# Performance work log

Hardware: AMD Instinct MI355X
Metric: run time of the kernel (lower is better)

## Reference

```python
import jax, jax.numpy as jnp
import numpy as np

N = 100000   # nodes
E = 1600000  # edges
R = 500      # relation types
D = 128      # in_ent_feats == out_ent_feats
H = 8        # heads
Dh = 16      # head dim
DFF = 4 * D  # feed-forward hidden
HOPS = 5
ALPHA = 0.15
SLOPE = 0.2
EPS = 1e-5


def setup_inputs() -> dict:
    key = jax.random.key(0)
    ks = jax.random.split(key, 12)
    s = 0.05  # small-init scale
    return {
        "ent_feat": jax.random.normal(ks[0], (N, D), jnp.float32),
        "rel_feat": jax.random.normal(ks[1], (R, D), jnp.float32),
        "src": jax.random.randint(ks[2], (E,), 0, N),
        "dst": jax.random.randint(ks[3], (E,), 0, N),
        "e_type": jax.random.randint(ks[4], (E,), 0, R),
        "ln1_g": jnp.ones((D,), jnp.float32),
        "ln1_b": jnp.zeros((D,), jnp.float32),
        "W_ent": jax.random.normal(ks[5], (D, H * Dh), jnp.float32) * s,
        "W_rel": jax.random.normal(ks[6], (D, H * Dh), jnp.float32) * s,
        "attn_h": jax.random.normal(ks[7], (1, H, Dh), jnp.float32) * s,
        "attn_t": jax.random.normal(ks[8], (1, H, Dh), jnp.float32) * s,
        "attn_r": jax.random.normal(ks[9], (1, H, Dh), jnp.float32) * s,
        "ln2_g": jnp.ones((H * Dh,), jnp.float32),
        "ln2_b": jnp.zeros((H * Dh,), jnp.float32),
        "W1": jax.random.normal(ks[10], (H * Dh, DFF), jnp.float32) * s,
        "b1": jnp.zeros((DFF,), jnp.float32),
        "W2": jax.random.normal(ks[11], (DFF, H * Dh), jnp.float32) * s,
        "b2": jnp.zeros((H * Dh,), jnp.float32),
    }


def _ln(x, g, b):
    mu = x.mean(-1, keepdims=True)
    var = x.var(-1, keepdims=True)
    return (x - mu) * jax.lax.rsqrt(var + EPS) * g + b


def reference(ent_feat, rel_feat, src, dst, e_type,
              ln1_g, ln1_b, W_ent, W_rel, attn_h, attn_t, attn_r,
              ln2_g, ln2_b, W1, b1, W2, b2):
    # graph layer norm (dropout is identity at eval)
    h = _ln(ent_feat, ln1_g, ln1_b)                       # [N, D]
    feat = (h @ W_ent).reshape(N, H, Dh)                  # [N, H, Dh]
    frel = (rel_feat @ W_rel).reshape(R, H, Dh)           # [R, H, Dh]
    eh = (feat * attn_h).sum(-1)                          # [N, H]
    et = (feat * attn_t).sum(-1)                          # [N, H]
    er = (frel * attn_r).sum(-1)[e_type]                  # [E, H]
    # edge scores: u_add_v + relation term, leaky relu
    e = eh[src] + et[dst] + er                            # [E, H]
    e = jnp.where(e > 0, e, SLOPE * e)
    # edge softmax over incoming edges of each dst node
    m = jax.ops.segment_max(e, dst, num_segments=N)       # [N, H]
    ex = jnp.exp(e - m[dst])
    ssum = jax.ops.segment_sum(ex, dst, num_segments=N)
    a = ex / ssum[dst]                                    # [E, H]
    # PPR diffusion
    feat0 = feat
    f = feat0
    for _ in range(HOPS):
        msg = f[src] * a[:, :, None]                      # [E, H, Dh]
        agg = jax.ops.segment_sum(msg, dst, num_segments=N)
        f = (1.0 - ALPHA) * agg + ALPHA * feat0
    # residual (Identity since in == out)
    rst = f + h.reshape(N, H, Dh)
    rst = rst.reshape(N, H * Dh)
    # feed-forward sublayer with residual
    y = _ln(rst, ln2_g, ln2_b)
    ff = jax.nn.relu(y @ W1 + b1) @ W2 + b2
    return ff + rst
```

## Files before the change

### kernel.cpp

```cpp
#include <hip/hip_runtime.h>
#include <hip/hip_bf16.h>
#include <math.h>

#define N_NODES 100000
#define N_EDGES 1600000
#define N_REL   500
#define DIM     128
#define NHEAD   8
#define DFF     512
#define ALPHA   0.15f
#define SLOPE   0.2f
#define LN_EPS  1e-5f

#define SCHUNK   1024
#define NSCANBLK ((N_NODES + SCHUNK - 1) / SCHUNK)

typedef unsigned short u16;
typedef unsigned int   u32;

typedef __attribute__((ext_vector_type(8))) short  bf16x8;
typedef __attribute__((ext_vector_type(4))) float  f32x4;

__device__ __forceinline__ float bf2f(u16 u) {
    return __uint_as_float(((u32)u) << 16);
}
__device__ __forceinline__ u16 f2bf(float f) {
    __hip_bfloat16 b = __float2bfloat16(f);
    return *reinterpret_cast<u16*>(&b);
}
__device__ __forceinline__ u32 pack2(float a, float b) {
    return (u32)f2bf(a) | ((u32)f2bf(b) << 16);
}

__global__ void zero_k(int* __restrict__ p, int n) {
    int i = blockIdx.x * blockDim.x + threadIdx.x;
    if (i < n) p[i] = 0;
}

__global__ void swz1_k(const float* __restrict__ W1, u16* __restrict__ W1s) {
    const int i = blockIdx.x * 256 + threadIdx.x;
    const int k = i >> 9, n = i & 511;
    W1s[n * DIM + k] = f2bf(W1[i]);
}
__global__ void swz2_k(const float* __restrict__ W2, u16* __restrict__ W2s) {
    const int i = blockIdx.x * 256 + threadIdx.x;
    const int k = i >> 7, n = i & 127;
    W2s[n * DFF + k] = f2bf(W2[i]);
}
__global__ void swze_k(const float* __restrict__ W, u16* __restrict__ Ws) {
    const int i = blockIdx.x * 256 + threadIdx.x;
    const int k = i >> 7, n = i & 127;
    Ws[n * DIM + k] = f2bf(W[i]);
}

__global__ __launch_bounds__(128) void ln1_k(const float* __restrict__ x,
        const float* __restrict__ g, const float* __restrict__ b,
        float* __restrict__ h) {
    const int n = blockIdx.x, t = threadIdx.x;
    const float v = x[n * DIM + t];
    float s = v, q = v * v;
#pragma unroll
    for (int off = 32; off > 0; off >>= 1) {
        s += __shfl_xor(s, off, 64);
        q += __shfl_xor(q, off, 64);
    }
    __shared__ float ss[2], qq[2];
    if ((t & 63) == 0) { ss[t >> 6] = s; qq[t >> 6] = q; }
    __syncthreads();
    s = ss[0] + ss[1]; q = qq[0] + qq[1];
    const float mu  = s * (1.0f / 128.0f);
    const float var = q * (1.0f / 128.0f) - mu * mu;
    const float rs  = rsqrtf(fmaxf(var, 0.f) + LN_EPS);
    h[n * DIM + t] = (v - mu) * rs * g[t] + b[t];
}

#define HP 136
__global__ __launch_bounds__(256) void proj_k(const float* __restrict__ h,
        const u16* __restrict__ Wes,
        u16* __restrict__ feat0) {
    __shared__ u16 hsb[32 * HP];
    const int t   = threadIdx.x;
    const int n0b = blockIdx.x * 32;

    {
        const int sr = t >> 3;
        const int sc = (t & 7) * 16;
        const float* hrow = &h[(size_t)(n0b + sr) * DIM + sc];
        u16* drow = &hsb[sr * HP + sc];
#pragma unroll
        for (int i = 0; i < 4; ++i) {
            const float4 hv = ((const float4*)hrow)[i];
            ushort4 o;
            o.x = f2bf(hv.x); o.y = f2bf(hv.y); o.z = f2bf(hv.z); o.w = f2bf(hv.w);
            ((ushort4*)drow)[i] = o;
        }
    }
    __syncthreads();

    const int wv   = t >> 6;
    const int lane = t & 63;
    const int lm   = lane & 15;
    const int q4   = lane >> 4;
    const int mrow = (wv & 1) * 16;
    const int chalf = (wv >> 1) * 64;

    bf16x8 afr[4];
#pragma unroll
    for (int kt = 0; kt < 4; ++kt)
        afr[kt] = *(const bf16x8*)&hsb[(mrow + lm) * HP + kt * 32 + q4 * 8];

#pragma unroll
    for (int nt = 0; nt < 4; ++nt) {
        const int c0 = chalf + nt * 16;
        f32x4 acc = {0.f, 0.f, 0.f, 0.f};
#pragma unroll
        for (int kt = 0; kt < 4; ++kt) {
            const bf16x8 bfr = *(const bf16x8*)&Wes[(c0 + lm) * DIM + kt * 32 + q4 * 8];
            acc = __builtin_amdgcn_mfma_f32_16x16x32_bf16(afr[kt], bfr, acc, 0, 0, 0);
        }
#pragma unroll
        for (int r = 0; r < 4; ++r)
            feat0[(size_t)(n0b + mrow + q4 * 4 + r) * DIM + c0 + lm] = f2bf(acc[r]);
    }
}

__global__ __launch_bounds__(256) void eh_k(const u16* __restrict__ feat0,
        const float* __restrict__ attn_h, const float* __restrict__ attn_t,
        float* __restrict__ eh, float* __restrict__ et) {
    __shared__ float ahs[DIM], ats[DIM];
    const int t = threadIdx.x;
    if (t < DIM) { ahs[t] = attn_h[t]; ats[t] = attn_t[t]; }
    __syncthreads();
    const int idx  = blockIdx.x * 256 + t;
    const int n    = idx >> 3;
    const int head = idx & 7;
    const u16* fp = &feat0[(size_t)n * DIM + head * 16];
    float sh = 0.f, st = 0.f;
#pragma unroll
    for (int i = 0; i < 4; ++i) {
        const ushort4 f4 = ((const ushort4*)fp)[i];
        const int c = head * 16 + i * 4;
        sh += bf2f(f4.x) * ahs[c+0] + bf2f(f4.y) * ahs[c+1]
            + bf2f(f4.z) * ahs[c+2] + bf2f(f4.w) * ahs[c+3];
        st += bf2f(f4.x) * ats[c+0] + bf2f(f4.y) * ats[c+1]
            + bf2f(f4.z) * ats[c+2] + bf2f(f4.w) * ats[c+3];
    }
    eh[idx] = sh;
    et[idx] = st;
}

__global__ __launch_bounds__(128) void rel_k(const float* __restrict__ rel_feat,
        const float* __restrict__ W,
        const float* __restrict__ attn_r, float* __restrict__ er) {
    __shared__ float rf[DIM];
    __shared__ float pr[DIM];
    const int r = blockIdx.x, t = threadIdx.x;
    rf[t] = rel_feat[r * DIM + t];
    __syncthreads();
    float acc = 0.f;
    for (int d = 0; d < DIM; ++d) acc += rf[d] * W[d * DIM + t];
    pr[t] = acc * attn_r[t];
    __syncthreads();
    if (t < NHEAD) {
        float s = 0.f;
        for (int i = 0; i < 16; ++i) s += pr[t * 16 + i];
        er[r * NHEAD + t] = s;
    }
}

__global__ void count_k(const int* __restrict__ dst, int* __restrict__ counts) {
    int e = blockIdx.x * blockDim.x + threadIdx.x;
    if (e < N_EDGES) atomicAdd(&counts[dst[e]], 1);
}

__global__ __launch_bounds__(256) void scan1_k(const int* __restrict__ counts,
        int* __restrict__ offsets, int* __restrict__ blk_sums, int n) {
    __shared__ int wsum[4];
    const int t = threadIdx.x, lane = t & 63, wid = t >> 6;
    const int base = blockIdx.x * SCHUNK + t * 4;
    int v0 = 0, v1 = 0, v2 = 0, v3 = 0;
    if (base + 3 < n) {
        const int4 c4 = *(const int4*)&counts[base];
        v0 = c4.x; v1 = c4.y; v2 = c4.z; v3 = c4.w;
    } else {
        if (base + 0 < n) v0 = counts[base + 0];
        if (base + 1 < n) v1 = counts[base + 1];
        if (base + 2 < n) v2 = counts[base + 2];
        if (base + 3 < n) v3 = counts[base + 3];
    }
    const int s4 = v0 + v1 + v2 + v3;
    int incl = s4;
#pragma unroll
    for (int off = 1; off < 64; off <<= 1) {
        const int tt = __shfl_up(incl, off, 64);
        if (lane >= off) incl += tt;
    }
    if (lane == 63) wsum[wid] = incl;
    __syncthreads();
    int wbase = 0;
#pragma unroll
    for (int w = 0; w < 4; ++w) if (w < wid) wbase += wsum[w];
    const int excl = wbase + incl - s4;
    if (base + 0 < n) offsets[base + 0] = excl;
    if (base + 1 < n) offsets[base + 1] = excl + v0;
    if (base + 2 < n) offsets[base + 2] = excl + v0 + v1;
    if (base + 3 < n) offsets[base + 3] = excl + v0 + v1 + v2;
    if (t == 255) blk_sums[blockIdx.x] = wbase + incl;
}

__global__ __launch_bounds__(128) void scan2_k(const int* __restrict__ blk_sums,
        int* __restrict__ blk_off, int* __restrict__ offsets, int nblk, int n) {
    const int t = threadIdx.x;
    const int v = (t < nblk) ? blk_sums[t] : 0;
    int incl = v;
#pragma unroll
    for (int off = 1; off < 64; off <<= 1) {
        const int tt = __shfl_up(incl, off, 64);
        if ((t & 63) >= off) incl += tt;
    }
    __shared__ int w0sum;
    if (t == 63) w0sum = incl;
    __syncthreads();
    int x = incl - v;
    if (t >= 64) x += w0sum;
    if (t < nblk) blk_off[t] = x;
    if (t == nblk - 1) offsets[n] = x + v;
}

__global__ __launch_bounds__(256) void scan3_k(int* __restrict__ offsets,
        int* __restrict__ cursor, const int* __restrict__ blk_off, int n) {
    const int add  = blk_off[blockIdx.x];
    const int base = blockIdx.x * SCHUNK + threadIdx.x * 4;
#pragma unroll
    for (int j = 0; j < 4; ++j) {
        const int i = base + j;
        if (i < n) {
            const int o = offsets[i] + add;
            offsets[i] = o;
            cursor[i]  = o;
        }
    }
}

__global__ void scatter_k(const int* __restrict__ src, const int* __restrict__ dst,
        const int* __restrict__ etype,
        const float* __restrict__ eh, const float* __restrict__ et,
        const float* __restrict__ er,
        int* __restrict__ cursor, int* __restrict__ csr_src,
        u16* __restrict__ csr_ab) {
    const int e = blockIdx.x * blockDim.x + threadIdx.x;
    if (e >= N_EDGES) return;
    const int s = src[e], d = dst[e], r = etype[e];
    const float4 h0 = *(const float4*)&eh[s * NHEAD];
    const float4 h1 = *(const float4*)&eh[s * NHEAD + 4];
    const float4 t0 = *(const float4*)&et[d * NHEAD];
    const float4 t1 = *(const float4*)&et[d * NHEAD + 4];
    const float4 r0 = *(const float4*)&er[r * NHEAD];
    const float4 r1 = *(const float4*)&er[r * NHEAD + 4];
    float4 a0, a1;
    a0.x = h0.x + t0.x + r0.x; a0.y = h0.y + t0.y + r0.y;
    a0.z = h0.z + t0.z + r0.z; a0.w = h0.w + t0.w + r0.w;
    a1.x = h1.x + t1.x + r1.x; a1.y = h1.y + t1.y + r1.y;
    a1.z = h1.z + t1.z + r1.z; a1.w = h1.w + t1.w + r1.w;
    a0.x = a0.x > 0.f ? a0.x : SLOPE * a0.x;
    a0.y = a0.y > 0.f ? a0.y : SLOPE * a0.y;
    a0.z = a0.z > 0.f ? a0.z : SLOPE * a0.z;
    a0.w = a0.w > 0.f ? a0.w : SLOPE * a0.w;
    a1.x = a1.x > 0.f ? a1.x : SLOPE * a1.x;
    a1.y = a1.y > 0.f ? a1.y : SLOPE * a1.y;
    a1.z = a1.z > 0.f ? a1.z : SLOPE * a1.z;
    a1.w = a1.w > 0.f ? a1.w : SLOPE * a1.w;
    const int pos = atomicAdd(&cursor[d], 1);
    if (pos < 0 || pos >= N_EDGES) return;
    csr_src[pos] = s;
    uint4 packed;
    packed.x = pack2(a0.x, a0.y);
    packed.y = pack2(a0.z, a0.w);
    packed.z = pack2(a1.x, a1.y);
    packed.w = pack2(a1.z, a1.w);
    *(uint4*)&csr_ab[(size_t)pos * NHEAD] = packed;
}

__global__ __launch_bounds__(256) void softmax_k(const int* __restrict__ offsets,
        u16* __restrict__ csr_ab, float* __restrict__ inv_buf) {
    const int n = blockIdx.x * 4 + (threadIdx.x >> 6);
    const int beg = offsets[n], end = offsets[n + 1];
    const int lane = threadIdx.x & 63;
    const int k  = lane & 7;
    const int eo = lane >> 3;
    float m = -1e30f;
    for (int e = beg + eo; e < end; e += 8)
        m = fmaxf(m, bf2f(csr_ab[(size_t)e * NHEAD + k]));
    m = fmaxf(m, __shfl_xor(m, 8, 64));
    m = fmaxf(m, __shfl_xor(m, 16, 64));
    m = fmaxf(m, __shfl_xor(m, 32, 64));
    float ssum = 0.f;
    for (int e = beg + eo; e < end; e += 8) {
        const float ex = expf(bf2f(csr_ab[(size_t)e * NHEAD + k]) - m);
        csr_ab[(size_t)e * NHEAD + k] = f2bf(ex);
        ssum += ex;
    }
    ssum += __shfl_xor(ssum, 8, 64);
    ssum += __shfl_xor(ssum, 16, 64);
    ssum += __shfl_xor(ssum, 32, 64);
    const float inv = 1.f / fmaxf(ssum, 1e-20f);
    if (lane < 8) inv_buf[n * NHEAD + lane] = inv;
}

__global__ __launch_bounds__(256) void hop_k(const u16* f_in,
        u16* __restrict__ f_out, const u16* feat0,
        const int* __restrict__ offsets, const int* __restrict__ csr_src,
        const u16* __restrict__ csr_ab, const float* __restrict__ inv_buf) {
    const int n    = blockIdx.x * 4 + (threadIdx.x >> 6);
    const int lane = threadIdx.x & 63;
    const int beg = offsets[n], end = offsets[n + 1];
    const int hsel = lane >> 3;
    const int d2   = lane << 1;
    float2 acc = {0.f, 0.f};
    int e = beg;
    for (; e + 4 <= end; e += 4) {
        const int s0 = csr_src[e + 0];
        const int s1 = csr_src[e + 1];
        const int s2 = csr_src[e + 2];
        const int s3 = csr_src[e + 3];
        const float a0 = bf2f(csr_ab[(size_t)(e + 0) * NHEAD + hsel]);
        const float a1 = bf2f(csr_ab[(size_t)(e + 1) * NHEAD + hsel]);
        const float a2 = bf2f(csr_ab[(size_t)(e + 2) * NHEAD + hsel]);
        const float a3 = bf2f(csr_ab[(size_t)(e + 3) * NHEAD + hsel]);
        const ushort2 w0 = *(const ushort2*)&f_in[s0 * DIM + d2];
        const ushort2 w1 = *(const ushort2*)&f_in[s1 * DIM + d2];
        const ushort2 w2 = *(const ushort2*)&f_in[s2 * DIM + d2];
        const ushort2 w3 = *(const ushort2*)&f_in[s3 * DIM + d2];
        acc.x += a0 * bf2f(w0.x) + a1 * bf2f(w1.x) + a2 * bf2f(w2.x) + a3 * bf2f(w3.x);
        acc.y += a0 * bf2f(w0.y) + a1 * bf2f(w1.y) + a2 * bf2f(w2.y) + a3 * bf2f(w3.y);
    }
    for (; e < end; ++e) {
        const int s0 = csr_src[e];
        const float a0 = bf2f(csr_ab[(size_t)e * NHEAD + hsel]);
        const ushort2 w0 = *(const ushort2*)&f_in[s0 * DIM + d2];
        acc.x += a0 * bf2f(w0.x);
        acc.y += a0 * bf2f(w0.y);
    }
    const float iv = inv_buf[n * NHEAD + hsel];
    const ushort2 p = *(const ushort2*)&feat0[n * DIM + d2];
    const float ox = (1.f - ALPHA) * acc.x * iv + ALPHA * bf2f(p.x);
    const float oy = (1.f - ALPHA) * acc.y * iv + ALPHA * bf2f(p.y);
    ushort2 o; o.x = f2bf(ox); o.y = f2bf(oy);
    *(ushort2*)&f_out[n * DIM + d2] = o;
}

#define YP 136
#define ZP 520
__global__ __launch_bounds__(256) void ffn_k(const u16* __restrict__ f,
        const float* __restrict__ h,
        const float* __restrict__ g2, const float* __restrict__ b2ln,
        const u16* __restrict__ W1s,
        const float* __restrict__ b1,
        const u16* __restrict__ W2s,
        const float* __restrict__ b2,
        float* __restrict__ out) {
    __shared__ u16 ysb[32 * YP];
    __shared__ u16 zsb[32 * ZP];
    __shared__ float red[32][8];
    __shared__ float red2[32][8];
    __shared__ float mu_s[32], rs_s[32];

    const int t   = threadIdx.x;
    const int n0b = blockIdx.x * 32;

    const int an = t >> 3;
    const int ap = t & 7;
    float rv[16];
    {
        const int gbase = (n0b + an) * DIM + ap * 16;
#pragma unroll
        for (int i = 0; i < 4; ++i) {
            const ushort4 fu = *(const ushort4*)&f[gbase + i * 4];
            const float4  hv = *(const float4*)&h[gbase + i * 4];
            rv[i * 4 + 0] = bf2f(fu.x) + hv.x;
            rv[i * 4 + 1] = bf2f(fu.y) + hv.y;
            rv[i * 4 + 2] = bf2f(fu.z) + hv.z;
            rv[i * 4 + 3] = bf2f(fu.w) + hv.w;
        }
        float s = 0.f, q = 0.f;
#pragma unroll
        for (int i = 0; i < 16; ++i) { s += rv[i]; q += rv[i] * rv[i]; }
        red[an][ap] = s; red2[an][ap] = q;
    }
    __syncthreads();
    if (t < 32) {
        float s = 0.f, q = 0.f;
#pragma unroll
        for (int i = 0; i < 8; ++i) { s += red[t][i]; q += red2[t][i]; }
        const float mu  = s * (1.0f / 128.0f);
        const float var = q * (1.0f / 128.0f) - mu * mu;
        mu_s[t] = mu;
        rs_s[t] = rsqrtf(fmaxf(var, 0.f) + LN_EPS);
    }
    __syncthreads();
    {
        const float mu = mu_s[an], rs = rs_s[an];
#pragma unroll
        for (int i = 0; i < 4; ++i) {
            ushort4 yo;
            const int c = ap * 16 + i * 4;
            yo.x = f2bf((rv[i*4+0] - mu) * rs * g2[c+0] + b2ln[c+0]);
            yo.y = f2bf((rv[i*4+1] - mu) * rs * g2[c+1] + b2ln[c+1]);
            yo.z = f2bf((rv[i*4+2] - mu) * rs * g2[c+2] + b2ln[c+2]);
            yo.w = f2bf((rv[i*4+3] - mu) * rs * g2[c+3] + b2ln[c+3]);
            *(ushort4*)&ysb[an * YP + c] = yo;
        }
    }
    __syncthreads();

    const int wv   = t >> 6;
    const int lane = t & 63;
    const int lm   = lane & 15;
    const int q4   = lane >> 4;

    bf16x8 afr[2][4];
#pragma unroll
    for (int mt = 0; mt < 2; ++mt)
#pragma unroll
        for (int kt = 0; kt < 4; ++kt)
            afr[mt][kt] = *(const bf16x8*)&ysb[(mt * 16 + lm) * YP + kt * 32 + q4 * 8];

    for (int nt = 0; nt < 8; ++nt) {
        const int n0 = wv * 128 + nt * 16;
        f32x4 acc0 = {0.f, 0.f, 0.f, 0.f};
        f32x4 acc1 = {0.f, 0.f, 0.f, 0.f};
#pragma unroll
        for (int kt = 0; kt < 4; ++kt) {
            const bf16x8 bfr = *(const bf16x8*)&W1s[(n0 + lm) * DIM + kt * 32 + q4 * 8];
            acc0 = __builtin_amdgcn_mfma_f32_16x16x32_bf16(afr[0][kt], bfr, acc0, 0, 0, 0);
            acc1 = __builtin_amdgcn_mfma_f32_16x16x32_bf16(afr[1][kt], bfr, acc1, 0, 0, 0);
        }
        const float bias = b1[n0 + lm];
#pragma unroll
        for (int r = 0; r < 4; ++r) {
            zsb[(q4 * 4 + r) * ZP + n0 + lm]        = f2bf(fmaxf(acc0[r] + bias, 0.f));
            zsb[(16 + q4 * 4 + r) * ZP + n0 + lm]   = f2bf(fmaxf(acc1[r] + bias, 0.f));
        }
    }
    __syncthreads();

    f32x4 acc[2][2];
#pragma unroll
    for (int i = 0; i < 2; ++i)
#pragma unroll
        for (int j = 0; j < 2; ++j)
            acc[i][j] = (f32x4){0.f, 0.f, 0.f, 0.f};
    const int c0 = wv * 32;
    for (int kt = 0; kt < 16; ++kt) {
        const bf16x8 a0 = *(const bf16x8*)&zsb[(lm) * ZP + kt * 32 + q4 * 8];
        const bf16x8 a1 = *(const bf16x8*)&zsb[(16 + lm) * ZP + kt * 32 + q4 * 8];
        const bf16x8 b0 = *(const bf16x8*)&W2s[(c0 + lm) * DFF + kt * 32 + q4 * 8];
        const bf16x8 b1f = *(const bf16x8*)&W2s[(c0 + 16 + lm) * DFF + kt * 32 + q4 * 8];
        acc[0][0] = __builtin_amdgcn_mfma_f32_16x16x32_bf16(a0, b0, acc[0][0], 0, 0, 0);
        acc[0][1] = __builtin_amdgcn_mfma_f32_16x16x32_bf16(a0, b1f, acc[0][1], 0, 0, 0);
        acc[1][0] = __builtin_amdgcn_mfma_f32_16x16x32_bf16(a1, b0, acc[1][0], 0, 0, 0);
        acc[1][1] = __builtin_amdgcn_mfma_f32_16x16x32_bf16(a1, b1f, acc[1][1], 0, 0, 0);
    }

#pragma unroll
    for (int ntile = 0; ntile < 2; ++ntile) {
        const int col = c0 + ntile * 16 + lm;
        const float bias = b2[col];
#pragma unroll
        for (int mt = 0; mt < 2; ++mt) {
#pragma unroll
            for (int r = 0; r < 4; ++r) {
                const int row  = mt * 16 + q4 * 4 + r;
                const int gidx = (n0b + row) * DIM + col;
                out[gidx] = acc[mt][ntile][r] + bias + bf2f(f[gidx]) + h[gidx];
            }
        }
    }
}

extern "C" void kernel_launch(void* const* d_in, const int* in_sizes, int n_in,
                              void* d_out, int out_size, void* d_ws, size_t ws_size,
                              hipStream_t stream) {
    const float* ent_feat = (const float*)d_in[0];
    const float* rel_feat = (const float*)d_in[1];
    const int*   src      = (const int*)d_in[2];
    const int*   dst      = (const int*)d_in[3];
    const int*   e_type   = (const int*)d_in[4];
    const float* ln1_g    = (const float*)d_in[5];
    const float* ln1_b    = (const float*)d_in[6];
    const float* W_ent    = (const float*)d_in[7];
    const float* W_rel    = (const float*)d_in[8];
    const float* attn_h   = (const float*)d_in[9];
    const float* attn_t   = (const float*)d_in[10];
    const float* attn_r   = (const float*)d_in[11];
    const float* ln2_g    = (const float*)d_in[12];
    const float* ln2_b    = (const float*)d_in[13];
    const float* W1       = (const float*)d_in[14];
    const float* b1       = (const float*)d_in[15];
    const float* W2       = (const float*)d_in[16];
    const float* b2       = (const float*)d_in[17];
    float* out = (float*)d_out;

    char* ws = (char*)d_ws;
    size_t used = 0;
    auto alloc = [&](size_t bytes) -> char* {
        char* p = ws + used;
        used += (bytes + 255) & ~(size_t)255;
        return p;
    };
    float* h       = (float*)alloc((size_t)N_NODES * DIM * 4);
    u16*   feat0   = (u16*)  alloc((size_t)N_NODES * DIM * 2);
    u16*   fA      = (u16*)  alloc((size_t)N_NODES * DIM * 2);
    u16*   fB      = (u16*)  alloc((size_t)N_NODES * DIM * 2);
    u16*   csr_ab  = (u16*)  alloc((size_t)N_EDGES * NHEAD * 2);
    float* eh      = (float*)alloc((size_t)N_NODES * NHEAD * 4);
    float* et      = (float*)alloc((size_t)N_NODES * NHEAD * 4);
    float* inv_buf = (float*)alloc((size_t)N_NODES * NHEAD * 4);
    int*   csr_src = (int*)  alloc((size_t)N_EDGES * 4);
    int*   counts  = (int*)  alloc((size_t)N_NODES * 4);
    int*   offsets = (int*)  alloc((size_t)(N_NODES + 1) * 4);
    int*   cursor  = (int*)  alloc((size_t)N_NODES * 4);
    float* er      = (float*)alloc((size_t)N_REL * NHEAD * 4);
    u16*   W1s     = (u16*)  alloc((size_t)DIM * DFF * 2);
    u16*   W2s     = (u16*)  alloc((size_t)DFF * DIM * 2);
    u16*   Wes     = (u16*)  alloc((size_t)DIM * DIM * 2);
    int*   blk_sums= (int*)  alloc((size_t)NSCANBLK * 4);
    int*   blk_off = (int*)  alloc((size_t)NSCANBLK * 4);

    if (used > ws_size) return;

    swz1_k<<<DIM * DFF / 256, 256, 0, stream>>>(W1, W1s);
    swz2_k<<<DFF * DIM / 256, 256, 0, stream>>>(W2, W2s);
    swze_k<<<DIM * DIM / 256, 256, 0, stream>>>(W_ent, Wes);

    ln1_k<<<N_NODES, 128, 0, stream>>>(ent_feat, ln1_g, ln1_b, h);
    proj_k<<<N_NODES / 32, 256, 0, stream>>>(h, Wes, feat0);
    eh_k<<<N_NODES * NHEAD / 256, 256, 0, stream>>>(feat0, attn_h, attn_t, eh, et);
    rel_k<<<N_REL, 128, 0, stream>>>(rel_feat, W_rel, attn_r, er);

    zero_k<<<(N_NODES + 255) / 256, 256, 0, stream>>>(counts, N_NODES);
    count_k<<<(N_EDGES + 255) / 256, 256, 0, stream>>>(dst, counts);
    scan1_k<<<NSCANBLK, 256, 0, stream>>>(counts, offsets, blk_sums, N_NODES);
    scan2_k<<<1, 128, 0, stream>>>(blk_sums, blk_off, offsets, NSCANBLK, N_NODES);
    scan3_k<<<NSCANBLK, 256, 0, stream>>>(offsets, cursor, blk_off, N_NODES);
    scatter_k<<<(N_EDGES + 255) / 256, 256, 0, stream>>>(src, dst, e_type, eh, et, er,
                                                         cursor, csr_src, csr_ab);
    softmax_k<<<N_NODES / 4, 256, 0, stream>>>(offsets, csr_ab, inv_buf);

    hop_k<<<N_NODES / 4, 256, 0, stream>>>(feat0, fA, feat0, offsets, csr_src, csr_ab, inv_buf);
    hop_k<<<N_NODES / 4, 256, 0, stream>>>(fA, fB, feat0, offsets, csr_src, csr_ab, inv_buf);
    hop_k<<<N_NODES / 4, 256, 0, stream>>>(fB, fA, feat0, offsets, csr_src, csr_ab, inv_buf);
    hop_k<<<N_NODES / 4, 256, 0, stream>>>(fA, fB, feat0, offsets, csr_src, csr_ab, inv_buf);
    hop_k<<<N_NODES / 4, 256, 0, stream>>>(fB, fA, feat0, offsets, csr_src, csr_ab, inv_buf);

    ffn_k<<<N_NODES / 32, 256, 0, stream>>>(fA, h, ln2_g, ln2_b, W1s, b1, W2s, b2,
                                            out);
}
```

Measured before the change: 954.7 us.

## Store LN1 output as bf16 and move edge score computation into softmax

The layer-norm output h is now written as bf16 rather than fp32, which halves its traffic in the projection and FFN kernels but rounds the residual added at the end. The scatter kernel now only writes edge ids into CSR order. The softmax kernel gathers src, etype, eh and er per edge, recomputing the scores in both passes, and writes csr_src. This drops the scattered 16-byte score writes from scatter but adds indirect gathers, read twice, in softmax.

```diff
diff --git a/kernel.cpp b/kernel.cpp
--- a/kernel.cpp
+++ b/kernel.cpp
@@ -28,9 +28,6 @@
     __hip_bfloat16 b = __float2bfloat16(f);
     return *reinterpret_cast<u16*>(&b);
 }
-__device__ __forceinline__ u32 pack2(float a, float b) {
-    return (u32)f2bf(a) | ((u32)f2bf(b) << 16);
-}
 
 __global__ void zero_k(int* __restrict__ p, int n) {
     int i = blockIdx.x * blockDim.x + threadIdx.x;
@@ -55,7 +52,7 @@
 
 __global__ __launch_bounds__(128) void ln1_k(const float* __restrict__ x,
         const float* __restrict__ g, const float* __restrict__ b,
-        float* __restrict__ h) {
+        u16* __restrict__ h) {
     const int n = blockIdx.x, t = threadIdx.x;
     const float v = x[n * DIM + t];
     float s = v, q = v * v;
@@ -71,11 +68,11 @@
     const float mu  = s * (1.0f / 128.0f);
     const float var = q * (1.0f / 128.0f) - mu * mu;
     const float rs  = rsqrtf(fmaxf(var, 0.f) + LN_EPS);
-    h[n * DIM + t] = (v - mu) * rs * g[t] + b[t];
+    h[n * DIM + t] = f2bf((v - mu) * rs * g[t] + b[t]);
 }
 
 #define HP 136
-__global__ __launch_bounds__(256) void proj_k(const float* __restrict__ h,
+__global__ __launch_bounds__(256) void proj_k(const u16* __restrict__ h,
         const u16* __restrict__ Wes,
         u16* __restrict__ feat0) {
     __shared__ u16 hsb[32 * HP];
@@ -85,15 +82,9 @@
     {
         const int sr = t >> 3;
         const int sc = (t & 7) * 16;
-        const float* hrow = &h[(size_t)(n0b + sr) * DIM + sc];
-        u16* drow = &hsb[sr * HP + sc];
-#pragma unroll
-        for (int i = 0; i < 4; ++i) {
-            const float4 hv = ((const float4*)hrow)[i];
-            ushort4 o;
-            o.x = f2bf(hv.x); o.y = f2bf(hv.y); o.z = f2bf(hv.z); o.w = f2bf(hv.w);
-            ((ushort4*)drow)[i] = o;
-        }
+        const u16* hrow = &h[(size_t)(n0b + sr) * DIM + sc];
+        *(uint4*)&hsb[sr * HP + sc]     = *(const uint4*)hrow;
+        *(uint4*)&hsb[sr * HP + sc + 8] = *(const uint4*)(hrow + 8);
     }
     __syncthreads();
 
@@ -242,62 +233,50 @@
     }
 }
 
-__global__ void scatter_k(const int* __restrict__ src, const int* __restrict__ dst,
-        const int* __restrict__ etype,
+__global__ void scatter_k(const int* __restrict__ dst,
+        int* __restrict__ cursor, int* __restrict__ csr_eid) {
+    const int e = blockIdx.x * blockDim.x + threadIdx.x;
+    if (e >= N_EDGES) return;
+    const int pos = atomicAdd(&cursor[dst[e]], 1);
+    if (pos < 0 || pos >= N_EDGES) return;
+    csr_eid[pos] = e;
+}
+
+__global__ __launch_bounds__(256) void softmax_k(const int* __restrict__ offsets,
+        const int* __restrict__ csr_eid,
+        const int* __restrict__ src, const int* __restrict__ etype,
         const float* __restrict__ eh, const float* __restrict__ et,
         const float* __restrict__ er,
-        int* __restrict__ cursor, int* __restrict__ csr_src,
-        u16* __restrict__ csr_ab) {
-    const int e = blockIdx.x * blockDim.x + threadIdx.x;
-    if (e >= N_EDGES) return;
-    const int s = src[e], d = dst[e], r = etype[e];
-    const float4 h0 = *(const float4*)&eh[s * NHEAD];
-    const float4 h1 = *(const float4*)&eh[s * NHEAD + 4];
-    const float4 t0 = *(const float4*)&et[d * NHEAD];
-    const float4 t1 = *(const float4*)&et[d * NHEAD + 4];
-    const float4 r0 = *(const float4*)&er[r * NHEAD];
-    const float4 r1 = *(const float4*)&er[r * NHEAD + 4];
-    float4 a0, a1;
-    a0.x = h0.x + t0.x + r0.x; a0.y = h0.y + t0.y + r0.y;
-    a0.z = h0.z + t0.z + r0.z; a0.w = h0.w + t0.w + r0.w;
-    a1.x = h1.x + t1.x + r1.x; a1.y = h1.y + t1.y + r1.y;
-    a1.z = h1.z + t1.z + r1.z; a1.w = h1.w + t1.w + r1.w;
-    a0.x = a0.x > 0.f ? a0.x : SLOPE * a0.x;
-    a0.y = a0.y > 0.f ? a0.y : SLOPE * a0.y;
-    a0.z = a0.z > 0.f ? a0.z : SLOPE * a0.z;
-    a0.w = a0.w > 0.f ? a0.w : SLOPE * a0.w;
-    a1.x = a1.x > 0.f ? a1.x : SLOPE * a1.x;
-    a1.y = a1.y > 0.f ? a1.y : SLOPE * a1.y;
-    a1.z = a1.z > 0.f ? a1.z : SLOPE * a1.z;
-    a1.w = a1.w > 0.f ? a1.w : SLOPE * a1.w;
-    const int pos = atomicAdd(&cursor[d], 1);
-    if (pos < 0 || pos >= N_EDGES) return;
-    csr_src[pos] = s;
-    uint4 packed;
-    packed.x = pack2(a0.x, a0.y);
-    packed.y = pack2(a0.z, a0.w);
-    packed.z = pack2(a1.x, a1.y);
-    packed.w = pack2(a1.z, a1.w);
-    *(uint4*)&csr_ab[(size_t)pos * NHEAD] = packed;
-}
-
-__global__ __launch_bounds__(256) void softmax_k(const int* __restrict__ offsets,
-        u16* __restrict__ csr_ab, float* __restrict__ inv_buf) {
+        int* __restrict__ csr_src, u16* __restrict__ csr_ab,
+        float* __restrict__ inv_buf) {
     const int n = blockIdx.x * 4 + (threadIdx.x >> 6);
     const int beg = offsets[n], end = offsets[n + 1];
     const int lane = threadIdx.x & 63;
     const int k  = lane & 7;
     const int eo = lane >> 3;
+    const float etv = et[n * NHEAD + k];
+
     float m = -1e30f;
-    for (int e = beg + eo; e < end; e += 8)
-        m = fmaxf(m, bf2f(csr_ab[(size_t)e * NHEAD + k]));
+    for (int e = beg + eo; e < end; e += 8) {
+        const int eid = csr_eid[e];
+        const int s = src[eid], r = etype[eid];
+        float sc = eh[s * NHEAD + k] + etv + er[r * NHEAD + k];
+        sc = sc > 0.f ? sc : SLOPE * sc;
+        m = fmaxf(m, sc);
+    }
     m = fmaxf(m, __shfl_xor(m, 8, 64));
     m = fmaxf(m, __shfl_xor(m, 16, 64));
     m = fmaxf(m, __shfl_xor(m, 32, 64));
+
     float ssum = 0.f;
     for (int e = beg + eo; e < end; e += 8) {
-        const float ex = expf(bf2f(csr_ab[(size_t)e * NHEAD + k]) - m);
+        const int eid = csr_eid[e];
+        const int s = src[eid], r = etype[eid];
+        float sc = eh[s * NHEAD + k] + etv + er[r * NHEAD + k];
+        sc = sc > 0.f ? sc : SLOPE * sc;
+        const float ex = expf(sc - m);
         csr_ab[(size_t)e * NHEAD + k] = f2bf(ex);
+        if (k == 0) csr_src[e] = s;
         ssum += ex;
     }
     ssum += __shfl_xor(ssum, 8, 64);
@@ -352,7 +331,7 @@
 #define YP 136
 #define ZP 520
 __global__ __launch_bounds__(256) void ffn_k(const u16* __restrict__ f,
-        const float* __restrict__ h,
+        const u16* __restrict__ h,
         const float* __restrict__ g2, const float* __restrict__ b2ln,
         const u16* __restrict__ W1s,
         const float* __restrict__ b1,
@@ -376,11 +355,11 @@
 #pragma unroll
         for (int i = 0; i < 4; ++i) {
             const ushort4 fu = *(const ushort4*)&f[gbase + i * 4];
-            const float4  hv = *(const float4*)&h[gbase + i * 4];
-            rv[i * 4 + 0] = bf2f(fu.x) + hv.x;
-            rv[i * 4 + 1] = bf2f(fu.y) + hv.y;
-            rv[i * 4 + 2] = bf2f(fu.z) + hv.z;
-            rv[i * 4 + 3] = bf2f(fu.w) + hv.w;
+            const ushort4 hv = *(const ushort4*)&h[gbase + i * 4];
+            rv[i * 4 + 0] = bf2f(fu.x) + bf2f(hv.x);
+            rv[i * 4 + 1] = bf2f(fu.y) + bf2f(hv.y);
+            rv[i * 4 + 2] = bf2f(fu.z) + bf2f(hv.z);
+            rv[i * 4 + 3] = bf2f(fu.w) + bf2f(hv.w);
         }
         float s = 0.f, q = 0.f;
 #pragma unroll
@@ -472,7 +451,7 @@
             for (int r = 0; r < 4; ++r) {
                 const int row  = mt * 16 + q4 * 4 + r;
                 const int gidx = (n0b + row) * DIM + col;
-                out[gidx] = acc[mt][ntile][r] + bias + bf2f(f[gidx]) + h[gidx];
+                out[gidx] = acc[mt][ntile][r] + bias + bf2f(f[gidx]) + bf2f(h[gidx]);
             }
         }
     }
@@ -508,7 +487,7 @@
         used += (bytes + 255) & ~(size_t)255;
         return p;
     };
-    float* h       = (float*)alloc((size_t)N_NODES * DIM * 4);
+    u16*   h       = (u16*)  alloc((size_t)N_NODES * DIM * 2);
     u16*   feat0   = (u16*)  alloc((size_t)N_NODES * DIM * 2);
     u16*   fA      = (u16*)  alloc((size_t)N_NODES * DIM * 2);
     u16*   fB      = (u16*)  alloc((size_t)N_NODES * DIM * 2);
@@ -517,6 +496,7 @@
     float* et      = (float*)alloc((size_t)N_NODES * NHEAD * 4);
     float* inv_buf = (float*)alloc((size_t)N_NODES * NHEAD * 4);
     int*   csr_src = (int*)  alloc((size_t)N_EDGES * 4);
+    int*   csr_eid = (int*)  alloc((size_t)N_EDGES * 4);
     int*   counts  = (int*)  alloc((size_t)N_NODES * 4);
     int*   offsets = (int*)  alloc((size_t)(N_NODES + 1) * 4);
     int*   cursor  = (int*)  alloc((size_t)N_NODES * 4);
@@ -543,9 +523,9 @@
     scan1_k<<<NSCANBLK, 256, 0, stream>>>(counts, offsets, blk_sums, N_NODES);
     scan2_k<<<1, 128, 0, stream>>>(blk_sums, blk_off, offsets, NSCANBLK, N_NODES);
     scan3_k<<<NSCANBLK, 256, 0, stream>>>(offsets, cursor, blk_off, N_NODES);
-    scatter_k<<<(N_EDGES + 255) / 256, 256, 0, stream>>>(src, dst, e_type, eh, et, er,
-                                                         cursor, csr_src, csr_ab);
-    softmax_k<<<N_NODES / 4, 256, 0, stream>>>(offsets, csr_ab, inv_buf);
+    scatter_k<<<(N_EDGES + 255) / 256, 256, 0, stream>>>(dst, cursor, csr_eid);
+    softmax_k<<<N_NODES / 4, 256, 0, stream>>>(offsets, csr_eid, src, e_type,
+                                               eh, et, er, csr_src, csr_ab, inv_buf);
 
     hop_k<<<N_NODES / 4, 256, 0, stream>>>(feat0, fA, feat0, offsets, csr_src, csr_ab, inv_buf);
     hop_k<<<N_NODES / 4, 256, 0, stream>>>(fA, fB, feat0, offsets, csr_src, csr_ab, inv_buf);
```

After: 1.012 ms. 6.0% more time.
